# Kernel tuning notes

Hardware: AMD Instinct MI355X
Metric: run time of the kernel (lower is better)

Reference implementation:

```python
import jax, jax.numpy as jnp
import numpy as np

B, H, S, DK, DV = 2, 16, 2048, 64, 64

def setup_inputs() -> dict:
    key = jax.random.key(0)
    kq, kk, kv, km = jax.random.split(key, 4)
    q = jax.random.normal(kq, (B, H, S, DK), dtype=jnp.float32)
    k = jax.random.normal(kk, (B, H, S, DK), dtype=jnp.float32)
    v = jax.random.normal(kv, (B, H, S, DV), dtype=jnp.float32)
    mask = jax.random.randint(km, (B, H, S, S), 0, 2).astype(jnp.bool_)
    return {"q": q, "k": k, "v": v, "mask": mask}

def reference(q, k, v, mask):
    d_k = q.shape[-1]
    # scores: [B, H, Sq, Sk]
    scores = jnp.einsum('bhqd,bhkd->bhqk', q, k) / np.sqrt(d_k).astype(jnp.float32)
    scores = jnp.where(mask, jnp.float32(-1e9), scores)
    attn = jax.nn.softmax(scores, axis=-1)
    return jnp.einsum('bhqk,bhkd->bhqd', attn, v)
```

## Files before the change

### kernel.cpp

```cpp
#include <hip/hip_runtime.h>


#define LOG2E 1.4426950408889634f
#define QSCALE (0.125f * LOG2E)

typedef __attribute__((ext_vector_type(8))) short short8;
typedef __attribute__((ext_vector_type(4))) short short4v;
typedef __attribute__((ext_vector_type(4))) float f32x4;
typedef unsigned __attribute__((ext_vector_type(4))) uintv4;

constexpr int S = 2048, D = 64;

__device__ __forceinline__ short bf16rne(float x) {
  union { float f; unsigned u; } cv; cv.f = x;
  unsigned u = cv.u;
  u += 0x7fffu + ((u >> 16) & 1u);
  return (short)(u >> 16);
}

__device__ __forceinline__ void glds16(const void* g, void* l) {
  __builtin_amdgcn_global_load_lds(
      (const __attribute__((address_space(1))) void*)g,
      (__attribute__((address_space(3))) void*)l, 16, 0, 0);
}

__global__ void prep(const float* __restrict__ kp, const float* __restrict__ vp,
                     short* __restrict__ kb, short* __restrict__ vt,
                     const unsigned* __restrict__ m, int* __restrict__ flag) {
  const int b = blockIdx.x;
  const int tid = threadIdx.x;
  if (b == 0 && tid < 64) {
    unsigned v = m[tid];
    unsigned long long big = __ballot(v > 1u && v != 0x3F800000u);
    unsigned long long isf = __ballot(v == 0x3F800000u);
    if (tid == 0) *flag = (big != 0ull && isf == 0ull) ? 1 : 0;
  }
  if (b < 2048) {
    size_t i = ((size_t)b * 256 + tid) * 8;
    float4 a = *(const float4*)(kp + i);
    float4 c = *(const float4*)(kp + i + 4);
    short8 s;
    s[0] = bf16rne(a.x); s[1] = bf16rne(a.y); s[2] = bf16rne(a.z); s[3] = bf16rne(a.w);
    s[4] = bf16rne(c.x); s[5] = bf16rne(c.y); s[6] = bf16rne(c.z); s[7] = bf16rne(c.w);
    *(short8*)&kb[i] = s;
  } else {
    __shared__ float tile[64][65];
    const int bb = b - 2048;
    const int bh = bb >> 5, k0 = (bb & 31) * 64;
    const float* src = vp + ((size_t)(bh * S + k0)) * D;
#pragma unroll
    for (int i = 0; i < 4; ++i) {
      int row = i * 16 + (tid >> 4);
      int col = (tid & 15) * 4;
      float4 x = *(const float4*)(src + row * D + col);
      tile[row][col] = x.x; tile[row][col + 1] = x.y;
      tile[row][col + 2] = x.z; tile[row][col + 3] = x.w;
    }
    __syncthreads();
#pragma unroll
    for (int i = 0; i < 4; ++i) {
      int dim = i * 16 + (tid >> 4);
      int kb4 = (tid & 15) * 4;
      short4v s;
#pragma unroll
      for (int j = 0; j < 4; ++j) s[j] = bf16rne(tile[kb4 + j][dim]);
      *(short4v*)&vt[((size_t)(bh * D + dim)) * S + k0 + kb4] = s;
    }
  }
}

__launch_bounds__(256, 2)
__global__ void attn_fwd(const float* __restrict__ qp, const short* __restrict__ kb,
                         const short* __restrict__ vt, const void* __restrict__ mp,
                         float* __restrict__ op, const int* __restrict__ fmtp) {
  const int fmt  = *fmtp;
  const int tid  = threadIdx.x;
  const int lane = tid & 63;
  const int w    = tid >> 6;
  const int c    = lane & 15;
  const int quad = lane >> 4;

  const int bid = (blockIdx.x & 7) * 64 + (blockIdx.x >> 3);
  const int bh  = bid >> 4;
  const int q0  = (bid & 15) * 128;

  __shared__ short ks[2][64 * 64];
  __shared__ short vs[2][64 * 64];

  short8 qB[2][2];
#pragma unroll
  for (int qg = 0; qg < 2; ++qg) {
    const float* qg_p = qp + ((size_t)(bh * S + q0 + w * 32 + qg * 16 + c)) * D;
#pragma unroll
    for (int kk = 0; kk < 2; ++kk) {
      const float* p = qg_p + kk * 32 + quad * 8;
      float4 x = *(const float4*)(p);
      float4 y = *(const float4*)(p + 4);
      short8 f;
      f[0] = bf16rne(x.x * QSCALE); f[1] = bf16rne(x.y * QSCALE);
      f[2] = bf16rne(x.z * QSCALE); f[3] = bf16rne(x.w * QSCALE);
      f[4] = bf16rne(y.x * QSCALE); f[5] = bf16rne(y.y * QSCALE);
      f[6] = bf16rne(y.z * QSCALE); f[7] = bf16rne(y.w * QSCALE);
      qB[qg][kk] = f;
    }
  }

  f32x4 O[2][4];
#pragma unroll
  for (int qg = 0; qg < 2; ++qg)
#pragma unroll
    for (int dt = 0; dt < 4; ++dt) O[qg][dt] = (f32x4){0.f, 0.f, 0.f, 0.f};
  float Lp[2] = {0.f, 0.f};

  const int rsub = lane >> 3;
  const int csw  = (lane & 7) ^ rsub;
  const short* kbase = kb + ((size_t)(bh * S)) * D;
  const short* vbase = vt + ((size_t)(bh * D)) * S;

  const size_t mro0 = ((size_t)(bh * S + q0 + w * 32 + c)) * S;
  const size_t mro1 = mro0 + (size_t)16 * S;

  unsigned long long mm[2][2];

  auto stage = [&](int it, int buf) {
    const int k0 = it * 64;
#pragma unroll
    for (int h2 = 0; h2 < 2; ++h2) {
      const int row = (h2 * 4 + w) * 8 + rsub;
      glds16(kbase + (size_t)(k0 + row) * 64 + csw * 8,
             (char*)&ks[buf][0] + (h2 * 4 + w) * 1024);
      glds16(vbase + (size_t)row * S + k0 + csw * 8,
             (char*)&vs[buf][0] + (h2 * 4 + w) * 1024);
    }
  };

  auto mload = [&](int it) {
    const int kO = it * 64;
    if (fmt == 1) {
#pragma unroll
      for (int qg = 0; qg < 2; ++qg)
#pragma unroll
        for (int kg = 0; kg < 2; ++kg)
          mm[qg][kg] = __builtin_nontemporal_load((const unsigned long long*)
              ((const unsigned char*)mp + (qg ? mro1 : mro0) + kO + kg * 32 + 8 * quad));
    } else {
#pragma unroll
      for (int qg = 0; qg < 2; ++qg)
#pragma unroll
        for (int kg = 0; kg < 2; ++kg) {
          const unsigned* m0 =
              (const unsigned*)mp + (qg ? mro1 : mro0) + kO + kg * 32 + 8 * quad;
          uintv4 a = __builtin_nontemporal_load((const uintv4*)m0);
          uintv4 b = __builtin_nontemporal_load((const uintv4*)(m0 + 4));
          unsigned long long t = 0ull;
#pragma unroll
          for (int j = 0; j < 4; ++j) {
            if (a[j]) t |= 0xffull << (8 * j);
            if (b[j]) t |= 0xffull << (8 * (j + 4));
          }
          mm[qg][kg] = t;
        }
    }
  };

  stage(0, 0);
  mload(0);

  for (int it = 0; it < 32; ++it) {
    const int buf = it & 1;
    __syncthreads();

    if (it + 1 < 32) stage(it + 1, buf ^ 1);

    unsigned long long mb[2][2];
#pragma unroll
    for (int qg = 0; qg < 2; ++qg) {
      mb[qg][0] = mm[qg][0]; mb[qg][1] = mm[qg][1];
    }
    if (it + 1 < 32) mload(it + 1);

#pragma unroll
    for (int kg = 0; kg < 2; ++kg) {
      short8 ka[2][2];
#pragma unroll
      for (int kt = 0; kt < 2; ++kt) {
        const int rr = kg * 32 + 8 * (c >> 2) + (c & 3) + 4 * kt;
        const int r7 = (c & 3) + 4 * kt;
#pragma unroll
        for (int kk = 0; kk < 2; ++kk)
          ka[kt][kk] = *(const short8*)&ks[buf][rr * 64 + (((kk * 4 + quad) ^ r7) * 8)];
      }
      short8 vb[4];
#pragma unroll
      for (int dt = 0; dt < 4; ++dt)
        vb[dt] = *(const short8*)&vs[buf][(dt * 16 + c) * 64 +
                                          (((kg * 4 + quad) ^ (c & 7)) * 8)];

#pragma unroll
      for (int qg = 0; qg < 2; ++qg) {
        f32x4 z0 = (f32x4){0.f, 0.f, 0.f, 0.f};
        f32x4 z1 = (f32x4){0.f, 0.f, 0.f, 0.f};
        z0 = __builtin_amdgcn_mfma_f32_16x16x32_bf16(ka[0][0], qB[qg][0], z0, 0, 0, 0);
        z0 = __builtin_amdgcn_mfma_f32_16x16x32_bf16(ka[0][1], qB[qg][1], z0, 0, 0, 0);
        z1 = __builtin_amdgcn_mfma_f32_16x16x32_bf16(ka[1][0], qB[qg][0], z1, 0, 0, 0);
        z1 = __builtin_amdgcn_mfma_f32_16x16x32_bf16(ka[1][1], qB[qg][1], z1, 0, 0, 0);

        short8 pf;
        float part = 0.f;
        const unsigned long long mq = mb[qg][kg];
#pragma unroll
        for (int j = 0; j < 8; ++j) {
          float zv = (j < 4) ? z0[j & 3] : z1[j & 3];
          float e = ((mq >> (8 * j)) & 0xffull) ? 0.f : exp2f(zv);
          part += e;
          pf[j] = bf16rne(e);
        }
        Lp[qg] += part;

#pragma unroll
        for (int dt = 0; dt < 4; ++dt)
          O[qg][dt] =
              __builtin_amdgcn_mfma_f32_16x16x32_bf16(pf, vb[dt], O[qg][dt], 0, 0, 0);
      }
    }
  }

#pragma unroll
  for (int qg = 0; qg < 2; ++qg) {
    float t = Lp[qg];
    t += __shfl_xor(t, 16);
    t += __shfl_xor(t, 32);
#pragma unroll
    for (int r = 0; r < 4; ++r) {
      float Ls = __shfl(t, (lane & 48) | (quad * 4 + r));
      float inv = 1.f / Ls;
      const size_t ob =
          ((size_t)(bh * S + q0 + w * 32 + qg * 16 + quad * 4 + r)) * D;
#pragma unroll
      for (int dt = 0; dt < 4; ++dt) op[ob + dt * 16 + c] = O[qg][dt][r] * inv;
    }
  }
}

extern "C" void kernel_launch(void* const* d_in, const int* in_sizes, int n_in,
                              void* d_out, int out_size, void* d_ws, size_t ws_size,
                              hipStream_t stream) {
  const float* q = (const float*)d_in[0];
  const float* k = (const float*)d_in[1];
  const float* v = (const float*)d_in[2];
  const void*  m = d_in[3];

  short* kbuf = (short*)d_ws;
  short* vtb  = (short*)((char*)d_ws + (8u << 20));
  int* flag   = (int*)((char*)d_ws + (16u << 20));

  prep<<<3072, 256, 0, stream>>>(k, v, kbuf, vtb, (const unsigned*)m, flag);
  attn_fwd<<<512, 256, 0, stream>>>(q, kbuf, vtb, m, (float*)d_out, flag);
}
```

Measured before the change: 775.7 us.

## Split key dimension across wave pairs and halve query tile to double grid

Each block now handles 64 query rows instead of 128. The four waves split as two query halves times two key halves. Each wave processes 32 keys of every 64-key tile, and partial O and L are reduced through shared memory at the end. The grid doubles to 1024 blocks and launch bounds raise occupancy to 4 blocks per CU, aiming for more parallelism and latency hiding. In exchange, every block reloads the full K/V stream, which doubles K/V traffic, and the end-of-kernel shared-memory reduction adds cost.

```diff
diff --git a/kernel.cpp b/kernel.cpp
--- a/kernel.cpp
+++ b/kernel.cpp
@@ -69,7 +69,7 @@
   }
 }
 
-__launch_bounds__(256, 2)
+__launch_bounds__(256, 4)
 __global__ void attn_fwd(const float* __restrict__ qp, const short* __restrict__ kb,
                          const short* __restrict__ vt, const void* __restrict__ mp,
                          float* __restrict__ op, const int* __restrict__ fmtp) {
@@ -79,18 +79,23 @@
   const int w    = tid >> 6;
   const int c    = lane & 15;
   const int quad = lane >> 4;
-
-  const int bid = (blockIdx.x & 7) * 64 + (blockIdx.x >> 3);
-  const int bh  = bid >> 4;
-  const int q0  = (bid & 15) * 128;
-
-  __shared__ short ks[2][64 * 64];
-  __shared__ short vs[2][64 * 64];
+  const int kh   = w & 1;
+  const int qh   = w >> 1;
+
+  const int bid = (blockIdx.x & 7) * 128 + (blockIdx.x >> 3);
+  const int bh  = bid >> 5;
+  const int q0  = (bid & 31) * 64;
+
+  __shared__ __align__(16) char smem[32768];
+  short* ksb = (short*)smem;
+  short* vsb = (short*)(smem + 16384);
+  float* Osc = (float*)smem;
+  float* Lsc = (float*)(smem + 17000);
 
   short8 qB[2][2];
 #pragma unroll
   for (int qg = 0; qg < 2; ++qg) {
-    const float* qg_p = qp + ((size_t)(bh * S + q0 + w * 32 + qg * 16 + c)) * D;
+    const float* qg_p = qp + ((size_t)(bh * S + q0 + qh * 32 + qg * 16 + c)) * D;
 #pragma unroll
     for (int kk = 0; kk < 2; ++kk) {
       const float* p = qg_p + kk * 32 + quad * 8;
@@ -117,10 +122,10 @@
   const short* kbase = kb + ((size_t)(bh * S)) * D;
   const short* vbase = vt + ((size_t)(bh * D)) * S;
 
-  const size_t mro0 = ((size_t)(bh * S + q0 + w * 32 + c)) * S;
+  const size_t mro0 = ((size_t)(bh * S + q0 + qh * 32 + c)) * S;
   const size_t mro1 = mro0 + (size_t)16 * S;
 
-  unsigned long long mm[2][2];
+  unsigned long long mm[2];
 
   auto stage = [&](int it, int buf) {
     const int k0 = it * 64;
@@ -128,38 +133,33 @@
     for (int h2 = 0; h2 < 2; ++h2) {
       const int row = (h2 * 4 + w) * 8 + rsub;
       glds16(kbase + (size_t)(k0 + row) * 64 + csw * 8,
-             (char*)&ks[buf][0] + (h2 * 4 + w) * 1024);
+             (char*)&ksb[buf * 4096] + (h2 * 4 + w) * 1024);
       glds16(vbase + (size_t)row * S + k0 + csw * 8,
-             (char*)&vs[buf][0] + (h2 * 4 + w) * 1024);
+             (char*)&vsb[buf * 4096] + (h2 * 4 + w) * 1024);
     }
   };
 
   auto mload = [&](int it) {
-    const int kO = it * 64;
+    const int kO = it * 64 + kh * 32;
     if (fmt == 1) {
 #pragma unroll
       for (int qg = 0; qg < 2; ++qg)
-#pragma unroll
-        for (int kg = 0; kg < 2; ++kg)
-          mm[qg][kg] = __builtin_nontemporal_load((const unsigned long long*)
-              ((const unsigned char*)mp + (qg ? mro1 : mro0) + kO + kg * 32 + 8 * quad));
+        mm[qg] = __builtin_nontemporal_load((const unsigned long long*)
+            ((const unsigned char*)mp + (qg ? mro1 : mro0) + kO + 8 * quad));
     } else {
 #pragma unroll
-      for (int qg = 0; qg < 2; ++qg)
-#pragma unroll
-        for (int kg = 0; kg < 2; ++kg) {
-          const unsigned* m0 =
-              (const unsigned*)mp + (qg ? mro1 : mro0) + kO + kg * 32 + 8 * quad;
-          uintv4 a = __builtin_nontemporal_load((const uintv4*)m0);
-          uintv4 b = __builtin_nontemporal_load((const uintv4*)(m0 + 4));
-          unsigned long long t = 0ull;
-#pragma unroll
-          for (int j = 0; j < 4; ++j) {
-            if (a[j]) t |= 0xffull << (8 * j);
-            if (b[j]) t |= 0xffull << (8 * (j + 4));
-          }
-          mm[qg][kg] = t;
+      for (int qg = 0; qg < 2; ++qg) {
+        const unsigned* m0 = (const unsigned*)mp + (qg ? mro1 : mro0) + kO + 8 * quad;
+        uintv4 a = __builtin_nontemporal_load((const uintv4*)m0);
+        uintv4 b = __builtin_nontemporal_load((const uintv4*)(m0 + 4));
+        unsigned long long t = 0ull;
+#pragma unroll
+        for (int j = 0; j < 4; ++j) {
+          if (a[j]) t |= 0xffull << (8 * j);
+          if (b[j]) t |= 0xffull << (8 * (j + 4));
         }
+        mm[qg] = t;
+      }
     }
   };
 
@@ -172,73 +172,92 @@
 
     if (it + 1 < 32) stage(it + 1, buf ^ 1);
 
-    unsigned long long mb[2][2];
+    unsigned long long mb0 = mm[0], mb1 = mm[1];
+    if (it + 1 < 32) mload(it + 1);
+
+    short8 ka[2][2];
+#pragma unroll
+    for (int kt = 0; kt < 2; ++kt) {
+      const int rr = kh * 32 + 8 * (c >> 2) + (c & 3) + 4 * kt;
+      const int r7 = (c & 3) + 4 * kt;
+#pragma unroll
+      for (int kk = 0; kk < 2; ++kk)
+        ka[kt][kk] =
+            *(const short8*)&ksb[buf * 4096 + rr * 64 + (((kk * 4 + quad) ^ r7) * 8)];
+    }
+    short8 vb[4];
+#pragma unroll
+    for (int dt = 0; dt < 4; ++dt)
+      vb[dt] = *(const short8*)&vsb[buf * 4096 + (dt * 16 + c) * 64 +
+                                    (((kh * 4 + quad) ^ (c & 7)) * 8)];
+
 #pragma unroll
     for (int qg = 0; qg < 2; ++qg) {
-      mb[qg][0] = mm[qg][0]; mb[qg][1] = mm[qg][1];
-    }
-    if (it + 1 < 32) mload(it + 1);
-
-#pragma unroll
-    for (int kg = 0; kg < 2; ++kg) {
-      short8 ka[2][2];
-#pragma unroll
-      for (int kt = 0; kt < 2; ++kt) {
-        const int rr = kg * 32 + 8 * (c >> 2) + (c & 3) + 4 * kt;
-        const int r7 = (c & 3) + 4 * kt;
-#pragma unroll
-        for (int kk = 0; kk < 2; ++kk)
-          ka[kt][kk] = *(const short8*)&ks[buf][rr * 64 + (((kk * 4 + quad) ^ r7) * 8)];
+      f32x4 z0 = (f32x4){0.f, 0.f, 0.f, 0.f};
+      f32x4 z1 = (f32x4){0.f, 0.f, 0.f, 0.f};
+      z0 = __builtin_amdgcn_mfma_f32_16x16x32_bf16(ka[0][0], qB[qg][0], z0, 0, 0, 0);
+      z0 = __builtin_amdgcn_mfma_f32_16x16x32_bf16(ka[0][1], qB[qg][1], z0, 0, 0, 0);
+      z1 = __builtin_amdgcn_mfma_f32_16x16x32_bf16(ka[1][0], qB[qg][0], z1, 0, 0, 0);
+      z1 = __builtin_amdgcn_mfma_f32_16x16x32_bf16(ka[1][1], qB[qg][1], z1, 0, 0, 0);
+
+      short8 pf;
+      float part = 0.f;
+      const unsigned long long mq = qg ? mb1 : mb0;
+#pragma unroll
+      for (int j = 0; j < 8; ++j) {
+        float zv = (j < 4) ? z0[j & 3] : z1[j & 3];
+        float e = ((mq >> (8 * j)) & 0xffull) ? 0.f : exp2f(zv);
+        part += e;
+        pf[j] = bf16rne(e);
       }
-      short8 vb[4];
+      Lp[qg] += part;
+
 #pragma unroll
       for (int dt = 0; dt < 4; ++dt)
-        vb[dt] = *(const short8*)&vs[buf][(dt * 16 + c) * 64 +
-                                          (((kg * 4 + quad) ^ (c & 7)) * 8)];
-
-#pragma unroll
-      for (int qg = 0; qg < 2; ++qg) {
-        f32x4 z0 = (f32x4){0.f, 0.f, 0.f, 0.f};
-        f32x4 z1 = (f32x4){0.f, 0.f, 0.f, 0.f};
-        z0 = __builtin_amdgcn_mfma_f32_16x16x32_bf16(ka[0][0], qB[qg][0], z0, 0, 0, 0);
-        z0 = __builtin_amdgcn_mfma_f32_16x16x32_bf16(ka[0][1], qB[qg][1], z0, 0, 0, 0);
-        z1 = __builtin_amdgcn_mfma_f32_16x16x32_bf16(ka[1][0], qB[qg][0], z1, 0, 0, 0);
-        z1 = __builtin_amdgcn_mfma_f32_16x16x32_bf16(ka[1][1], qB[qg][1], z1, 0, 0, 0);
-
-        short8 pf;
-        float part = 0.f;
-        const unsigned long long mq = mb[qg][kg];
-#pragma unroll
-        for (int j = 0; j < 8; ++j) {
-          float zv = (j < 4) ? z0[j & 3] : z1[j & 3];
-          float e = ((mq >> (8 * j)) & 0xffull) ? 0.f : exp2f(zv);
-          part += e;
-          pf[j] = bf16rne(e);
-        }
-        Lp[qg] += part;
-
-#pragma unroll
-        for (int dt = 0; dt < 4; ++dt)
-          O[qg][dt] =
-              __builtin_amdgcn_mfma_f32_16x16x32_bf16(pf, vb[dt], O[qg][dt], 0, 0, 0);
-      }
-    }
-  }
-
+        O[qg][dt] =
+            __builtin_amdgcn_mfma_f32_16x16x32_bf16(pf, vb[dt], O[qg][dt], 0, 0, 0);
+    }
+  }
+
+  float Lq[2];
 #pragma unroll
   for (int qg = 0; qg < 2; ++qg) {
     float t = Lp[qg];
     t += __shfl_xor(t, 16);
     t += __shfl_xor(t, 32);
-#pragma unroll
-    for (int r = 0; r < 4; ++r) {
-      float Ls = __shfl(t, (lane & 48) | (quad * 4 + r));
-      float inv = 1.f / Ls;
-      const size_t ob =
-          ((size_t)(bh * S + q0 + w * 32 + qg * 16 + quad * 4 + r)) * D;
-#pragma unroll
-      for (int dt = 0; dt < 4; ++dt) op[ob + dt * 16 + c] = O[qg][dt][r] * inv;
-    }
+    Lq[qg] = t;
+  }
+
+  __syncthreads();
+  if (kh == 1) {
+#pragma unroll
+    for (int qg = 0; qg < 2; ++qg) {
+#pragma unroll
+      for (int dt = 0; dt < 4; ++dt)
+#pragma unroll
+        for (int r = 0; r < 4; ++r)
+          Osc[(qh * 32 + qg * 16 + quad * 4 + r) * 66 + dt * 16 + c] = O[qg][dt][r];
+    }
+    if (quad == 0) {
+      Lsc[qh * 32 + c]      = Lq[0];
+      Lsc[qh * 32 + 16 + c] = Lq[1];
+    }
+  }
+  __syncthreads();
+  if (kh == 0) {
+#pragma unroll
+    for (int qg = 0; qg < 2; ++qg)
+#pragma unroll
+      for (int r = 0; r < 4; ++r) {
+        const int qrow = qg * 16 + quad * 4 + r;
+        float Ls = __shfl(Lq[qg], (lane & 48) | (quad * 4 + r)) + Lsc[qh * 32 + qrow];
+        float inv = 1.f / Ls;
+        const size_t ob = ((size_t)(bh * S + q0 + qh * 32 + qrow)) * D;
+#pragma unroll
+        for (int dt = 0; dt < 4; ++dt)
+          op[ob + dt * 16 + c] =
+              (O[qg][dt][r] + Osc[(qh * 32 + qrow) * 66 + dt * 16 + c]) * inv;
+      }
   }
 }
 
@@ -255,5 +274,5 @@
   int* flag   = (int*)((char*)d_ws + (16u << 20));
 
   prep<<<3072, 256, 0, stream>>>(k, v, kbuf, vtb, (const unsigned*)m, flag);
-  attn_fwd<<<512, 256, 0, stream>>>(q, kbuf, vtb, m, (float*)d_out, flag);
-}
+  attn_fwd<<<1024, 256, 0, stream>>>(q, kbuf, vtb, m, (float*)d_out, flag);
+}
```

Result: no change. 787.3 us (+1.5%).
